# Kernel optimization log

Measured on AMD Instinct MI355X. Metric: run time of the kernel, lower is better.

The kernel has to match this reference:

```python
import jax, jax.numpy as jnp
import numpy as np

NUM_TOKENS = 2048
HIDDEN = 2048
MOE_INTER = 1408
N_EXPERTS = 16
TOP_K = 4
N_SHARED = 2
SHARED_INTER = N_SHARED * MOE_INTER  # 2816
CAPACITY = 768
ROUTED_SCALE = 1.0


def setup_inputs() -> dict:
    key = jax.random.key(0)
    ks = jax.random.split(key, 9)
    s = 0.02  # init scale for stability
    return {
        "hidden_states": jax.random.normal(ks[0], (NUM_TOKENS, HIDDEN), jnp.float32),
        "w_gate": jax.random.normal(ks[1], (N_EXPERTS, HIDDEN), jnp.float32) * s,
        "w1": jax.random.normal(ks[2], (N_EXPERTS, HIDDEN, MOE_INTER), jnp.float32) * s,  # gate_proj
        "w3": jax.random.normal(ks[3], (N_EXPERTS, HIDDEN, MOE_INTER), jnp.float32) * s,  # up_proj
        "w2": jax.random.normal(ks[4], (N_EXPERTS, MOE_INTER, HIDDEN), jnp.float32) * s,  # down_proj
        "ws1": jax.random.normal(ks[5], (HIDDEN, SHARED_INTER), jnp.float32) * s,
        "ws3": jax.random.normal(ks[6], (HIDDEN, SHARED_INTER), jnp.float32) * s,
        "ws2": jax.random.normal(ks[7], (SHARED_INTER, HIDDEN), jnp.float32) * s,
    }


def _moe_forward(x, w_gate, w1, w3, w2, ws1, ws3, ws2):
    T, d = x.shape
    E = w1.shape[0]
    # ---- router: softmax scores, top-k selection (DeepSeek-V2, norm_topk_prob=False) ----
    scores = jax.nn.softmax(x @ w_gate.T, axis=-1)            # [T, E]
    topw, topi = jax.lax.top_k(scores, TOP_K)                 # [T, K]
    topw = topw * ROUTED_SCALE
    flat_e = topi.reshape(-1)                                 # [T*K] expert id per slot
    flat_w = topw.reshape(-1)                                 # [T*K]
    tok_ids = jnp.repeat(jnp.arange(T), TOP_K)                # [T*K]
    # ---- dispatch: position of each slot within its expert's buffer ----
    onehot = jax.nn.one_hot(flat_e, E, dtype=jnp.int32)       # [T*K, E]
    pos = jnp.take_along_axis(jnp.cumsum(onehot, axis=0), flat_e[:, None], axis=1)[:, 0] - 1
    valid = (pos < CAPACITY).astype(x.dtype)
    buf = jnp.zeros((E, CAPACITY, d), x.dtype).at[flat_e, pos].set(x[tok_ids], mode='drop')
    # ---- grouped SwiGLU expert FFN ----
    g = jnp.einsum('ecd,edi->eci', buf, w1)
    u = jnp.einsum('ecd,edi->eci', buf, w3)
    o = jnp.einsum('eci,eid->ecd', jax.nn.silu(g) * u, w2)    # [E, C, d]
    # ---- combine: gather back, weight, scatter-add per token ----
    gathered = o[flat_e, jnp.clip(pos, 0, CAPACITY - 1)] * (flat_w * valid)[:, None]
    routed = jax.ops.segment_sum(gathered, tok_ids, num_segments=T)  # [T, d]
    # ---- shared experts (always-on SwiGLU) ----
    shared = (jax.nn.silu(x @ ws1) * (x @ ws3)) @ ws2
    return routed + shared


def reference(hidden_states, w_gate, w1, w3, w2, ws1, ws3, ws2):
    return _moe_forward(hidden_states, w_gate, w1, w3, w2, ws1, ws3, ws2)
```

## Files before the change

### kernel.cpp

```cpp
#include <hip/hip_runtime.h>
#include <hip/hip_bf16.h>
#include <cstdint>

#define T_TOKENS 2048
#define HIDDEN 2048
#define INTER 1408
#define NEXP 16
#define TOPK 4
#define SINTER 2816
#define CAP 768
#define BK 32

typedef __attribute__((ext_vector_type(8))) short short8;
typedef __attribute__((ext_vector_type(8))) unsigned short ushort8;
typedef __attribute__((ext_vector_type(4))) float f32x4;

__device__ __forceinline__ float4 ld4f(const float* p) {
  return *reinterpret_cast<const float4*>(p);
}

__device__ __forceinline__ unsigned short f2bf(float v) {
  unsigned int u = __float_as_uint(v);
  unsigned int r = (u + 0x7FFFu + ((u >> 16) & 1u)) >> 16;
  return (unsigned short)r;
}

__device__ __forceinline__ void gld16(const void* g, void* l) {
  __builtin_amdgcn_global_load_lds(
      (const __attribute__((address_space(1))) void*)g,
      (__attribute__((address_space(3))) void*)l, 16, 0, 0);
}

__global__ __launch_bounds__(64) void router_kernel(
    const float* __restrict__ x, const float* __restrict__ wg,
    int* __restrict__ topi, float* __restrict__ topw)
{
  const int t = blockIdx.x;
  const int lane = threadIdx.x;
  float acc[NEXP];
#pragma unroll
  for (int e = 0; e < NEXP; ++e) acc[e] = 0.f;
  const float* xr = x + (size_t)t * HIDDEN;
  for (int i = lane; i < HIDDEN; i += 64) {
    float xv = xr[i];
#pragma unroll
    for (int e = 0; e < NEXP; ++e) acc[e] += xv * wg[e * HIDDEN + i];
  }
#pragma unroll
  for (int e = 0; e < NEXP; ++e) {
#pragma unroll
    for (int off = 32; off > 0; off >>= 1)
      acc[e] += __shfl_xor(acc[e], off);
  }
  float m = acc[0];
#pragma unroll
  for (int e = 1; e < NEXP; ++e) m = fmaxf(m, acc[e]);
  float p[NEXP];
  float s = 0.f;
#pragma unroll
  for (int e = 0; e < NEXP; ++e) { p[e] = expf(acc[e] - m); s += p[e]; }
  const float inv = 1.f / s;
#pragma unroll
  for (int e = 0; e < NEXP; ++e) p[e] *= inv;
  if (lane == 0) {
#pragma unroll
    for (int k = 0; k < TOPK; ++k) {
      float best = -1.f; int bi = 0;
#pragma unroll
      for (int e = 0; e < NEXP; ++e)
        if (p[e] > best) { best = p[e]; bi = e; }
      topi[t * TOPK + k] = bi;
      topw[t * TOPK + k] = best;
      p[bi] = -1.f;
    }
  }
}

__global__ __launch_bounds__(1024) void partition_kernel(
    const int* __restrict__ topi, float* __restrict__ topw,
    int* __restrict__ rowtok, int* __restrict__ count)
{
  __shared__ int se[T_TOKENS * TOPK];
  for (int i = threadIdx.x; i < T_TOKENS * TOPK; i += 1024) se[i] = topi[i];
  __syncthreads();

  const int wave = threadIdx.x >> 6;
  const int lane = threadIdx.x & 63;
  const uint64_t below = (lane == 0) ? 0ull : ((~0ull) >> (64 - lane));
  int base = 0;
  for (int c = 0; c < T_TOKENS * TOPK; c += 64) {
    int ev = se[c + lane];
    uint64_t mask = __ballot(ev == wave);
    if (ev == wave) {
      int my = base + __popcll(mask & below);
      if (my < CAP) rowtok[wave * CAP + my] = c + lane;
      else          topw[c + lane] = 0.f;
    }
    base += __popcll(mask);
  }
  if (lane == 0) count[wave] = base < CAP ? base : CAP;
}

__global__ __launch_bounds__(256) void cvt_x_kernel(
    const float* __restrict__ x, unsigned short* __restrict__ xb)
{
  const long i = ((long)blockIdx.x * 256 + threadIdx.x) * 8;
  float4 a = ld4f(x + i), b = ld4f(x + i + 4);
  float v[8] = {a.x, a.y, a.z, a.w, b.x, b.y, b.z, b.w};
  unsigned short o[8];
#pragma unroll
  for (int j = 0; j < 8; ++j) o[j] = f2bf(v[j]);
  *(ushort8*)(xb + i) = *(ushort8*)&o[0];
}

__device__ __forceinline__ void tcvt_body(
    int bx, int by, int bz,
    const float* W0, const float* W1, unsigned short* T,
    int K, int N, long tz, int mul, int nz0, int which0, int which1,
    float (*tile)[65])
{
  const float* W; int which; long zz;
  if (bz < nz0) { W = W0; which = which0; zz = bz; }
  else          { W = W1; which = which1; zz = bz - nz0; }
  W += zz * (long)K * N;
  T += zz * tz;
  const int k0 = bx * 64, n0 = by * 64;
  const int tr = threadIdx.x >> 4;
  const int tc4 = (threadIdx.x & 15) * 4;
#pragma unroll
  for (int p = 0; p < 4; ++p) {
    int r = p * 16 + tr;
    float4 v = ld4f(W + (long)(k0 + r) * N + n0 + tc4);
    tile[r][tc4] = v.x; tile[r][tc4 + 1] = v.y;
    tile[r][tc4 + 2] = v.z; tile[r][tc4 + 3] = v.w;
  }
  __syncthreads();
  const int wn = threadIdx.x >> 3;
  const int wk = (threadIdx.x & 7) * 8;
#pragma unroll
  for (int p = 0; p < 2; ++p) {
    int n = p * 32 + wn;
    unsigned short o[8];
#pragma unroll
    for (int j = 0; j < 8; ++j) o[j] = f2bf(tile[wk + j][n]);
    const int gn = n0 + n;
    const long prow = ((long)(gn >> 4) * mul + which) * 16 + (gn & 15);
    *(ushort8*)(T + prow * K + k0 + wk) = *(ushort8*)&o[0];
  }
}

__global__ __launch_bounds__(256) void tcvt_w_kernel(
    const float* __restrict__ W0, const float* __restrict__ W1,
    unsigned short* __restrict__ T,
    int K, int N, long tz, int mul, int nz0, int which0, int which1)
{
  __shared__ float tile[64][65];
  tcvt_body(blockIdx.x, blockIdx.y, blockIdx.z, W0, W1, T, K, N, tz, mul,
            nz0, which0, which1, tile);
}

template<int NW, int EPI>
__global__ __launch_bounds__(NW * 64, 2)
void gemm_bf(const unsigned short* __restrict__ Ag, int ldka,
             const unsigned short* __restrict__ Bg, long bstride,
             float* __restrict__ C, unsigned short* __restrict__ H, int ldc,
             const float* __restrict__ TW,
             const int* __restrict__ arows_g, int ashift, long aexp,
             const int* __restrict__ crows_g, long cexp,
             const int* __restrict__ cnt, int Mfix, int K,
             int MT, int NTn,
             const float* tW0, const float* tW1, unsigned short* tT,
             int tK, int tN, long ttz, int tmul, int tnz0, int tw0, int tw1,
             int tKX, int tNY, int gemmBlocks)
{
  constexpr int TN = NW * 32;
  constexpr int GA = 8 / NW;
  constexpr int WN = NW / 2;

  __shared__ __align__(16) unsigned short sA[3][128 * BK];
  __shared__ __align__(16) unsigned short sB[3][TN * BK];

  if ((int)blockIdx.x >= gemmBlocks) {
    const int tbid = (int)blockIdx.x - gemmBlocks;
    const int bx = tbid % tKX;
    const int rest2 = tbid / tKX;
    const int by = rest2 % tNY;
    const int bz = rest2 / tNY;
    tcvt_body(bx, by, bz, tW0, tW1, tT, tK, tN, ttz, tmul, tnz0, tw0, tw1,
              (float(*)[65])&sA[0][0]);
    return;
  }

  const int lin = (blockIdx.x & 7) * (gemmBlocks >> 3) + (blockIdx.x >> 3);
  const int mt = lin % MT;
  const int rest = lin / MT;
  const int nt = rest % NTn;
  const int e = rest / NTn;

  const int M = cnt ? cnt[e] : Mfix;
  if (mt * 128 >= M) return;
  const int n0 = nt * TN;

  const int tid = threadIdx.x;
  const int l = tid & 63;
  const int w = tid >> 6;
  const int wm = w / WN;
  const int wn = w % WN;
  const int fr = l & 15;
  const int fc = l >> 4;

  const int* arows = arows_g ? arows_g + e * CAP : nullptr;
  const int* crows = crows_g ? crows_g + e * CAP : nullptr;
  const unsigned short* Bexp = Bg + (long)e * bstride;

  const int rb_s = ((l >> 3) & 1) | (((l >> 5) & 1) << 1);
  const int sch = ((l & 3) ^ rb_s) * 8;
  long aoff[GA], boff[2];
#pragma unroll
  for (int j = 0; j < GA; ++j) {
    const int rloc = (w * GA + j) * 16 + (l >> 2);
    int r = mt * 128 + rloc;
    if (r > M - 1) r = M - 1;
    const long arow = arows ? (long)(arows[r] >> ashift) : (aexp * e + r);
    aoff[j] = arow * (long)ldka + sch;
  }
#pragma unroll
  for (int j = 0; j < 2; ++j) {
    const int rloc = (w * 2 + j) * 16 + (l >> 2);
    boff[j] = (long)(n0 + rloc) * K + sch;
  }

  const int rb_r = ((fr >> 1) & 1) | (((fr >> 3) & 1) << 1);
  const int pcoff = (fc ^ rb_r) * 8;

  f32x4 acc[4][4];
#pragma unroll
  for (int i = 0; i < 4; ++i)
#pragma unroll
    for (int j = 0; j < 4; ++j) acc[i][j] = (f32x4)0.f;

  const int NT = K / BK;

  auto stage = [&](int buf, int kt) {
#pragma unroll
    for (int j = 0; j < GA; ++j)
      gld16(Ag + aoff[j] + kt, &sA[buf][(w * GA + j) * 16 * BK]);
#pragma unroll
    for (int j = 0; j < 2; ++j)
      gld16(Bexp + boff[j] + kt, &sB[buf][(w * 2 + j) * 16 * BK]);
  };

  stage(0, 0);
  stage(1, BK);

  int rb = 0, wb = 2;
  for (int t = 0; t < NT; ++t) {
    if (t + 1 < NT) {
      if constexpr (NW == 8) asm volatile("s_waitcnt vmcnt(3)" ::: "memory");
      else                   asm volatile("s_waitcnt vmcnt(4)" ::: "memory");
    } else {
      asm volatile("s_waitcnt vmcnt(0)" ::: "memory");
    }
    __builtin_amdgcn_s_barrier();
    __builtin_amdgcn_sched_barrier(0);

    if (t + 2 < NT) stage(wb, (t + 2) * BK);

    short8 fa[4], fb[4];
#pragma unroll
    for (int mi = 0; mi < 4; ++mi)
      fa[mi] = *(const short8*)&sA[rb][(wm * 64 + mi * 16 + fr) * BK + pcoff];
#pragma unroll
    for (int ni = 0; ni < 4; ++ni)
      fb[ni] = *(const short8*)&sB[rb][(wn * 64 + ni * 16 + fr) * BK + pcoff];
#pragma unroll
    for (int mi = 0; mi < 4; ++mi)
#pragma unroll
      for (int ni = 0; ni < 4; ++ni)
        acc[mi][ni] = __builtin_amdgcn_mfma_f32_16x16x32_bf16(fa[mi], fb[ni], acc[mi][ni], 0, 0, 0);

    rb = (rb == 2) ? 0 : rb + 1;
    wb = (wb == 2) ? 0 : wb + 1;
  }

#pragma unroll
  for (int mi = 0; mi < 4; ++mi)
#pragma unroll
    for (int rr = 0; rr < 4; ++rr) {
      const int r = mt * 128 + wm * 64 + mi * 16 + fc * 4 + rr;
      if (r >= M) continue;
      if constexpr (EPI == 2) {
        const long crow = crows ? (long)crows[r] : (cexp * e + r);
#pragma unroll
        for (int np = 0; np < 2; ++np) {
          const float g = acc[mi][2 * np][rr];
          const float u = acc[mi][2 * np + 1][rr];
          const float h = u * (g / (1.f + __expf(-g)));
          const int i = (n0 / 32 + wn * 2 + np) * 16 + fr;
          H[crow * (long)ldc + i] = f2bf(h);
        }
      } else if constexpr (EPI == 3) {
        const int slot = crows[r];
        const float wgt = TW[slot];
        if (wgt != 0.f) {
          const long tok = slot >> 2;
#pragma unroll
          for (int ni = 0; ni < 4; ++ni) {
            const int col = n0 + wn * 64 + ni * 16 + fr;
            atomicAdd(&C[tok * (long)ldc + col], wgt * acc[mi][ni][rr]);
          }
        }
      } else {
        const long crow = crows ? (long)crows[r] : (cexp * e + r);
#pragma unroll
        for (int ni = 0; ni < 4; ++ni) {
          const int col = n0 + wn * 64 + ni * 16 + fr;
          C[crow * (long)ldc + col] = acc[mi][ni][rr];
        }
      }
    }
}

extern "C" void kernel_launch(void* const* d_in, const int* in_sizes, int n_in,
                              void* d_out, int out_size, void* d_ws, size_t ws_size,
                              hipStream_t stream)
{
  const float* x   = (const float*)d_in[0];
  const float* wg  = (const float*)d_in[1];
  const float* w1  = (const float*)d_in[2];
  const float* w3  = (const float*)d_in[3];
  const float* w2  = (const float*)d_in[4];
  const float* ws1 = (const float*)d_in[5];
  const float* ws3 = (const float*)d_in[6];
  const float* ws2 = (const float*)d_in[7];
  float* out = (float*)d_out;

  char* w = (char*)d_ws;
  int*   topi   = (int*)w;   w += (size_t)T_TOKENS * TOPK * 4;
  float* topw   = (float*)w; w += (size_t)T_TOKENS * TOPK * 4;
  int*   rowtok = (int*)w;   w += (size_t)NEXP * CAP * 4;
  int*   count  = (int*)w;   w += 256;
  uintptr_t a = (uintptr_t)w; a = (a + 255) & ~(uintptr_t)255; w = (char*)a;

  const size_t XSZ  = (size_t)T_TOKENS * HIDDEN;
  const size_t WSI  = (size_t)2 * HIDDEN * SINTER;
  const size_t WRI  = (size_t)2 * NEXP * HIDDEN * INTER;
  const size_t HSSZ = (size_t)T_TOKENS * SINTER;
  const size_t HRSZ = (size_t)NEXP * CAP * INTER;

  unsigned short* xb  = (unsigned short*)w; w += XSZ * 2;
  unsigned short* wSi = (unsigned short*)w; w += WSI * 2;
  unsigned short* wRi = (unsigned short*)w; w += WRI * 2;
  unsigned short* hs  = (unsigned short*)w; w += HSSZ * 2;
  unsigned short* hr  = (unsigned short*)w; w += HRSZ * 2;
  unsigned short* wS2 = wSi;
  unsigned short* wR2 = wRi;

  router_kernel<<<T_TOKENS, 64, 0, stream>>>(x, wg, topi, topw);
  partition_kernel<<<1, 1024, 0, stream>>>(topi, topw, rowtok, count);
  cvt_x_kernel<<<(int)(XSZ / (256 * 8)), 256, 0, stream>>>(x, xb);

  tcvt_w_kernel<<<dim3(HIDDEN / 64, SINTER / 64, 2), 256, 0, stream>>>(
      ws1, ws3, wSi, HIDDEN, SINTER, 0L, 2, 1, 0, 1);

  {
    const int G = (T_TOKENS / 128) * (2 * SINTER / 128);
    const int TCVT = (HIDDEN / 64) * (INTER / 64) * (2 * NEXP);
    gemm_bf<4, 2><<<G + TCVT, 256, 0, stream>>>(
        xb, HIDDEN, wSi, 0L, nullptr, hs, SINTER, nullptr,
        nullptr, 0, 0L, nullptr, 0L,
        nullptr, T_TOKENS, HIDDEN, T_TOKENS / 128, 2 * SINTER / 128,
        w1, w3, wRi, HIDDEN, INTER, (long)2 * HIDDEN * INTER, 2, NEXP, 0, 1,
        HIDDEN / 64, INTER / 64, G);
  }

  {
    const int G = (CAP / 128) * (2 * INTER / 128) * NEXP;
    const int TCVT = (SINTER / 64) * (HIDDEN / 64);
    gemm_bf<4, 2><<<G + TCVT, 256, 0, stream>>>(
        xb, HIDDEN, wRi, (long)2 * HIDDEN * INTER, nullptr, hr, INTER, nullptr,
        rowtok, 2, 0L, nullptr, (long)CAP,
        count, 0, HIDDEN, CAP / 128, 2 * INTER / 128,
        ws2, ws2, wS2, SINTER, HIDDEN, 0L, 1, 1, 0, 0,
        SINTER / 64, HIDDEN / 64, G);
  }

  {
    const int G = (T_TOKENS / 128) * (HIDDEN / 128);
    const int TCVT = (INTER / 64) * (HIDDEN / 64) * NEXP;
    gemm_bf<4, 0><<<G + TCVT, 256, 0, stream>>>(
        hs, SINTER, wS2, 0L, out, nullptr, HIDDEN, nullptr,
        nullptr, 0, 0L, nullptr, 0L,
        nullptr, T_TOKENS, SINTER, T_TOKENS / 128, HIDDEN / 128,
        w2, w2, wR2, INTER, HIDDEN, (long)INTER * HIDDEN, 1, NEXP, 0, 0,
        INTER / 64, HIDDEN / 64, G);
  }

  {
    const int G = (CAP / 128) * (HIDDEN / 128) * NEXP;
    gemm_bf<4, 3><<<G, 256, 0, stream>>>(
        hr, INTER, wR2, (long)INTER * HIDDEN, out, nullptr, HIDDEN, topw,
        nullptr, 0, (long)CAP, rowtok, 0L,
        count, 0, INTER, CAP / 128, HIDDEN / 128,
        nullptr, nullptr, nullptr, 1, 1, 0L, 1, 1, 0, 0,
        1, 1, G);
  }
}
```

Baseline: 583.8 us.

## Merge shared and routed down-projection GEMMs into one atomic-accumulating launch

```diff
diff --git a/kernel.cpp b/kernel.cpp
--- a/kernel.cpp
+++ b/kernel.cpp
@@ -159,75 +159,60 @@
             nz0, which0, which1, tile);
 }
 
-template<int NW, int EPI>
-__global__ __launch_bounds__(NW * 64, 2)
-void gemm_bf(const unsigned short* __restrict__ Ag, int ldka,
-             const unsigned short* __restrict__ Bg, long bstride,
-             float* __restrict__ C, unsigned short* __restrict__ H, int ldc,
-             const float* __restrict__ TW,
-             const int* __restrict__ arows_g, int ashift, long aexp,
-             const int* __restrict__ crows_g, long cexp,
-             const int* __restrict__ cnt, int Mfix, int K,
-             int MT, int NTn,
-             const float* tW0, const float* tW1, unsigned short* tT,
-             int tK, int tN, long ttz, int tmul, int tnz0, int tw0, int tw1,
-             int tKX, int tNY, int gemmBlocks)
-{
-  constexpr int TN = NW * 32;
-  constexpr int GA = 8 / NW;
-  constexpr int WN = NW / 2;
-
-  __shared__ __align__(16) unsigned short sA[3][128 * BK];
-  __shared__ __align__(16) unsigned short sB[3][TN * BK];
-
-  if ((int)blockIdx.x >= gemmBlocks) {
-    const int tbid = (int)blockIdx.x - gemmBlocks;
-    const int bx = tbid % tKX;
-    const int rest2 = tbid / tKX;
-    const int by = rest2 % tNY;
-    const int bz = rest2 / tNY;
-    tcvt_body(bx, by, bz, tW0, tW1, tT, tK, tN, ttz, tmul, tnz0, tw0, tw1,
-              (float(*)[65])&sA[0][0]);
-    return;
-  }
-
-  const int lin = (blockIdx.x & 7) * (gemmBlocks >> 3) + (blockIdx.x >> 3);
-  const int mt = lin % MT;
-  const int rest = lin / MT;
-  const int nt = rest % NTn;
-  const int e = rest / NTn;
-
-  const int M = cnt ? cnt[e] : Mfix;
+struct GemmCfg {
+  const unsigned short* Ag; int ldka;
+  const unsigned short* Bg; long bstride;
+  float* C; unsigned short* H; int ldc;
+  const float* TW;
+  const int* arows_g; int ashift; long aexp;
+  const int* crows_g; long cexp;
+  const int* cnt; int Mfix; int K; int MT; int NTn;
+  int epi;
+  int nblk;
+};
+
+struct TcvtCfg {
+  const float* W0; const float* W1; unsigned short* T;
+  int K, N; long tz; int mul, nz0, w0, w1, KX, NY, nblk;
+};
+
+__device__ __forceinline__ void gemm_run(const GemmCfg& c, int bid,
+                                         unsigned short* sA, unsigned short* sB)
+{
+  const int G = c.nblk;
+  const int lin = (bid & 7) * (G >> 3) + (bid >> 3);
+  const int mt = lin % c.MT;
+  const int rest = lin / c.MT;
+  const int nt = rest % c.NTn;
+  const int e = rest / c.NTn;
+
+  const int M = c.cnt ? c.cnt[e] : c.Mfix;
   if (mt * 128 >= M) return;
-  const int n0 = nt * TN;
+  const int n0 = nt * 128;
 
   const int tid = threadIdx.x;
   const int l = tid & 63;
   const int w = tid >> 6;
-  const int wm = w / WN;
-  const int wn = w % WN;
+  const int wm = w >> 1;
+  const int wn = w & 1;
   const int fr = l & 15;
   const int fc = l >> 4;
 
-  const int* arows = arows_g ? arows_g + e * CAP : nullptr;
-  const int* crows = crows_g ? crows_g + e * CAP : nullptr;
-  const unsigned short* Bexp = Bg + (long)e * bstride;
+  const int* arows = c.arows_g ? c.arows_g + e * CAP : nullptr;
+  const int* crows = c.crows_g ? c.crows_g + e * CAP : nullptr;
+  const unsigned short* Bexp = c.Bg + (long)e * c.bstride;
 
   const int rb_s = ((l >> 3) & 1) | (((l >> 5) & 1) << 1);
   const int sch = ((l & 3) ^ rb_s) * 8;
-  long aoff[GA], boff[2];
-#pragma unroll
-  for (int j = 0; j < GA; ++j) {
-    const int rloc = (w * GA + j) * 16 + (l >> 2);
+  long aoff[2], boff[2];
+#pragma unroll
+  for (int j = 0; j < 2; ++j) {
+    const int rloc = (w * 2 + j) * 16 + (l >> 2);
     int r = mt * 128 + rloc;
     if (r > M - 1) r = M - 1;
-    const long arow = arows ? (long)(arows[r] >> ashift) : (aexp * e + r);
-    aoff[j] = arow * (long)ldka + sch;
-  }
-#pragma unroll
-  for (int j = 0; j < 2; ++j) {
-    const int rloc = (w * 2 + j) * 16 + (l >> 2);
-    boff[j] = (long)(n0 + rloc) * K + sch;
+    const long arow = arows ? (long)(arows[r] >> c.ashift) : (c.aexp * e + r);
+    aoff[j] = arow * (long)c.ldka + sch;
+    boff[j] = (long)(n0 + rloc) * c.K + sch;
   }
 
   const int rb_r = ((fr >> 1) & 1) | (((fr >> 3) & 1) << 1);
@@ -239,15 +224,14 @@
 #pragma unroll
     for (int j = 0; j < 4; ++j) acc[i][j] = (f32x4)0.f;
 
-  const int NT = K / BK;
+  const int NT = c.K / BK;
 
   auto stage = [&](int buf, int kt) {
 #pragma unroll
-    for (int j = 0; j < GA; ++j)
-      gld16(Ag + aoff[j] + kt, &sA[buf][(w * GA + j) * 16 * BK]);
-#pragma unroll
-    for (int j = 0; j < 2; ++j)
-      gld16(Bexp + boff[j] + kt, &sB[buf][(w * 2 + j) * 16 * BK]);
+    for (int j = 0; j < 2; ++j) {
+      gld16(c.Ag + aoff[j] + kt, sA + buf * (128 * BK) + (w * 2 + j) * 16 * BK);
+      gld16(Bexp + boff[j] + kt, sB + buf * (128 * BK) + (w * 2 + j) * 16 * BK);
+    }
   };
 
   stage(0, 0);
@@ -255,12 +239,8 @@
 
   int rb = 0, wb = 2;
   for (int t = 0; t < NT; ++t) {
-    if (t + 1 < NT) {
-      if constexpr (NW == 8) asm volatile("s_waitcnt vmcnt(3)" ::: "memory");
-      else                   asm volatile("s_waitcnt vmcnt(4)" ::: "memory");
-    } else {
-      asm volatile("s_waitcnt vmcnt(0)" ::: "memory");
-    }
+    if (t + 1 < NT) asm volatile("s_waitcnt vmcnt(4)" ::: "memory");
+    else            asm volatile("s_waitcnt vmcnt(0)" ::: "memory");
     __builtin_amdgcn_s_barrier();
     __builtin_amdgcn_sched_barrier(0);
 
@@ -269,10 +249,10 @@
     short8 fa[4], fb[4];
 #pragma unroll
     for (int mi = 0; mi < 4; ++mi)
-      fa[mi] = *(const short8*)&sA[rb][(wm * 64 + mi * 16 + fr) * BK + pcoff];
+      fa[mi] = *(const short8*)(sA + rb * (128 * BK) + (wm * 64 + mi * 16 + fr) * BK + pcoff);
 #pragma unroll
     for (int ni = 0; ni < 4; ++ni)
-      fb[ni] = *(const short8*)&sB[rb][(wn * 64 + ni * 16 + fr) * BK + pcoff];
+      fb[ni] = *(const short8*)(sB + rb * (128 * BK) + (wn * 64 + ni * 16 + fr) * BK + pcoff);
 #pragma unroll
     for (int mi = 0; mi < 4; ++mi)
 #pragma unroll
@@ -289,36 +269,65 @@
     for (int rr = 0; rr < 4; ++rr) {
       const int r = mt * 128 + wm * 64 + mi * 16 + fc * 4 + rr;
       if (r >= M) continue;
-      if constexpr (EPI == 2) {
-        const long crow = crows ? (long)crows[r] : (cexp * e + r);
+      if (c.epi == 2) {
+        const long crow = crows ? (long)crows[r] : (c.cexp * e + r);
 #pragma unroll
         for (int np = 0; np < 2; ++np) {
           const float g = acc[mi][2 * np][rr];
           const float u = acc[mi][2 * np + 1][rr];
           const float h = u * (g / (1.f + __expf(-g)));
           const int i = (n0 / 32 + wn * 2 + np) * 16 + fr;
-          H[crow * (long)ldc + i] = f2bf(h);
+          c.H[crow * (long)c.ldc + i] = f2bf(h);
         }
-      } else if constexpr (EPI == 3) {
+      } else if (c.epi == 3) {
         const int slot = crows[r];
-        const float wgt = TW[slot];
+        const float wgt = c.TW[slot];
         if (wgt != 0.f) {
           const long tok = slot >> 2;
 #pragma unroll
           for (int ni = 0; ni < 4; ++ni) {
             const int col = n0 + wn * 64 + ni * 16 + fr;
-            atomicAdd(&C[tok * (long)ldc + col], wgt * acc[mi][ni][rr]);
+            atomicAdd(&c.C[tok * (long)c.ldc + col], wgt * acc[mi][ni][rr]);
           }
         }
-      } else {
-        const long crow = crows ? (long)crows[r] : (cexp * e + r);
+      } else if (c.epi == 4) {
+        const long crow = crows ? (long)crows[r] : (c.cexp * e + r);
 #pragma unroll
         for (int ni = 0; ni < 4; ++ni) {
           const int col = n0 + wn * 64 + ni * 16 + fr;
-          C[crow * (long)ldc + col] = acc[mi][ni][rr];
+          atomicAdd(&c.C[crow * (long)c.ldc + col], acc[mi][ni][rr]);
+        }
+      } else {
+        const long crow = crows ? (long)crows[r] : (c.cexp * e + r);
+#pragma unroll
+        for (int ni = 0; ni < 4; ++ni) {
+          const int col = n0 + wn * 64 + ni * 16 + fr;
+          c.C[crow * (long)c.ldc + col] = acc[mi][ni][rr];
         }
       }
     }
+}
+
+__global__ __launch_bounds__(256, 2)
+void mega_kernel(GemmCfg g1, GemmCfg g2, TcvtCfg t1, TcvtCfg t2)
+{
+  __shared__ __align__(16) unsigned short sA[3][128 * BK];
+  __shared__ __align__(16) unsigned short sB[3][128 * BK];
+
+  int bid = (int)blockIdx.x;
+  if (bid < g1.nblk) { gemm_run(g1, bid, &sA[0][0], &sB[0][0]); return; }
+  bid -= g1.nblk;
+  if (bid < g2.nblk) { gemm_run(g2, bid, &sA[0][0], &sB[0][0]); return; }
+  bid -= g2.nblk;
+  const TcvtCfg* tc;
+  if (bid < t1.nblk) { tc = &t1; }
+  else               { bid -= t1.nblk; tc = &t2; }
+  const int bx = bid % tc->KX;
+  const int rest = bid / tc->KX;
+  const int by = rest % tc->NY;
+  const int bz = rest / tc->NY;
+  tcvt_body(bx, by, bz, tc->W0, tc->W1, tc->T, tc->K, tc->N, tc->tz, tc->mul,
+            tc->nz0, tc->w0, tc->w1, (float(*)[65])&sA[0][0]);
 }
 
 extern "C" void kernel_launch(void* const* d_in, const int* in_sizes, int n_in,
@@ -345,64 +354,63 @@
   const size_t XSZ  = (size_t)T_TOKENS * HIDDEN;
   const size_t WSI  = (size_t)2 * HIDDEN * SINTER;
   const size_t WRI  = (size_t)2 * NEXP * HIDDEN * INTER;
+  const size_t WR2  = (size_t)NEXP * INTER * HIDDEN;
   const size_t HSSZ = (size_t)T_TOKENS * SINTER;
   const size_t HRSZ = (size_t)NEXP * CAP * INTER;
 
   unsigned short* xb  = (unsigned short*)w; w += XSZ * 2;
   unsigned short* wSi = (unsigned short*)w; w += WSI * 2;
   unsigned short* wRi = (unsigned short*)w; w += WRI * 2;
+  unsigned short* wR2 = (unsigned short*)w; w += WR2 * 2;
   unsigned short* hs  = (unsigned short*)w; w += HSSZ * 2;
   unsigned short* hr  = (unsigned short*)w; w += HRSZ * 2;
   unsigned short* wS2 = wSi;
-  unsigned short* wR2 = wRi;
+
+  hipMemsetAsync(out, 0, (size_t)T_TOKENS * HIDDEN * 4, stream);
 
   router_kernel<<<T_TOKENS, 64, 0, stream>>>(x, wg, topi, topw);
   partition_kernel<<<1, 1024, 0, stream>>>(topi, topw, rowtok, count);
   cvt_x_kernel<<<(int)(XSZ / (256 * 8)), 256, 0, stream>>>(x, xb);
 
+  GemmCfg gz = {}; TcvtCfg tz = {};
+
   tcvt_w_kernel<<<dim3(HIDDEN / 64, SINTER / 64, 2), 256, 0, stream>>>(
       ws1, ws3, wSi, HIDDEN, SINTER, 0L, 2, 1, 0, 1);
 
   {
-    const int G = (T_TOKENS / 128) * (2 * SINTER / 128);
-    const int TCVT = (HIDDEN / 64) * (INTER / 64) * (2 * NEXP);
-    gemm_bf<4, 2><<<G + TCVT, 256, 0, stream>>>(
-        xb, HIDDEN, wSi, 0L, nullptr, hs, SINTER, nullptr,
-        nullptr, 0, 0L, nullptr, 0L,
-        nullptr, T_TOKENS, HIDDEN, T_TOKENS / 128, 2 * SINTER / 128,
-        w1, w3, wRi, HIDDEN, INTER, (long)2 * HIDDEN * INTER, 2, NEXP, 0, 1,
-        HIDDEN / 64, INTER / 64, G);
+    GemmCfg g1 = { xb, HIDDEN, wSi, 0L, nullptr, hs, SINTER, nullptr,
+                   nullptr, 0, 0L, nullptr, 0L,
+                   nullptr, T_TOKENS, HIDDEN, T_TOKENS / 128, 2 * SINTER / 128,
+                   2, (T_TOKENS / 128) * (2 * SINTER / 128) };
+    TcvtCfg t1 = { w1, w3, wRi, HIDDEN, INTER, (long)2 * HIDDEN * INTER,
+                   2, NEXP, 0, 1, HIDDEN / 64, INTER / 64,
+                   (HIDDEN / 64) * (INTER / 64) * (2 * NEXP) };
+    mega_kernel<<<g1.nblk + t1.nblk, 256, 0, stream>>>(g1, gz, t1, tz);
   }
 
   {
-    const int G = (CAP / 128) * (2 * INTER / 128) * NEXP;
-    const int TCVT = (SINTER / 64) * (HIDDEN / 64);
-    gemm_bf<4, 2><<<G + TCVT, 256, 0, stream>>>(
-        xb, HIDDEN, wRi, (long)2 * HIDDEN * INTER, nullptr, hr, INTER, nullptr,
-        rowtok, 2, 0L, nullptr, (long)CAP,
-        count, 0, HIDDEN, CAP / 128, 2 * INTER / 128,
-        ws2, ws2, wS2, SINTER, HIDDEN, 0L, 1, 1, 0, 0,
-        SINTER / 64, HIDDEN / 64, G);
+    GemmCfg g1 = { xb, HIDDEN, wRi, (long)2 * HIDDEN * INTER, nullptr, hr, INTER, nullptr,
+                   rowtok, 2, 0L, nullptr, (long)CAP,
+                   count, 0, HIDDEN, CAP / 128, 2 * INTER / 128,
+                   2, (CAP / 128) * (2 * INTER / 128) * NEXP };
+    TcvtCfg t1 = { ws2, ws2, wS2, SINTER, HIDDEN, 0L,
+                   1, 1, 0, 0, SINTER / 64, HIDDEN / 64,
+                   (SINTER / 64) * (HIDDEN / 64) };
+    TcvtCfg t2 = { w2, w2, wR2, INTER, HIDDEN, (long)INTER * HIDDEN,
+                   1, NEXP, 0, 0, INTER / 64, HIDDEN / 64,
+                   (INTER / 64) * (HIDDEN / 64) * NEXP };
+    mega_kernel<<<g1.nblk + t1.nblk + t2.nblk, 256, 0, stream>>>(g1, gz, t1, t2);
   }
 
   {
-    const int G = (T_TOKENS / 128) * (HIDDEN / 128);
-    const int TCVT = (INTER / 64) * (HIDDEN / 64) * NEXP;
-    gemm_bf<4, 0><<<G + TCVT, 256, 0, stream>>>(
-        hs, SINTER, wS2, 0L, out, nullptr, HIDDEN, nullptr,
-        nullptr, 0, 0L, nullptr, 0L,
-        nullptr, T_TOKENS, SINTER, T_TOKENS / 128, HIDDEN / 128,
-        w2, w2, wR2, INTER, HIDDEN, (long)INTER * HIDDEN, 1, NEXP, 0, 0,
-        INTER / 64, HIDDEN / 64, G);
-  }
-
-  {
-    const int G = (CAP / 128) * (HIDDEN / 128) * NEXP;
-    gemm_bf<4, 3><<<G, 256, 0, stream>>>(
-        hr, INTER, wR2, (long)INTER * HIDDEN, out, nullptr, HIDDEN, topw,
-        nullptr, 0, (long)CAP, rowtok, 0L,
-        count, 0, INTER, CAP / 128, HIDDEN / 128,
-        nullptr, nullptr, nullptr, 1, 1, 0L, 1, 1, 0, 0,
-        1, 1, G);
-  }
-}
+    GemmCfg g1 = { hs, SINTER, wS2, 0L, out, nullptr, HIDDEN, nullptr,
+                   nullptr, 0, 0L, nullptr, 0L,
+                   nullptr, T_TOKENS, SINTER, T_TOKENS / 128, HIDDEN / 128,
+                   4, (T_TOKENS / 128) * (HIDDEN / 128) };
+    GemmCfg g2 = { hr, INTER, wR2, (long)INTER * HIDDEN, out, nullptr, HIDDEN, topw,
+                   nullptr, 0, (long)CAP, rowtok, 0L,
+                   count, 0, INTER, CAP / 128, HIDDEN / 128,
+                   3, (CAP / 128) * (HIDDEN / 128) * NEXP };
+    mega_kernel<<<g1.nblk + g2.nblk, 256, 0, stream>>>(g1, g2, tz, tz);
+  }
+}
```

After: 589.0 us. About the same (+0.9%).
